# Kernel tuning notes

Measured on AMD Instinct MI355X. Metric: run time of the kernel, lower is better.

The kernel has to match this reference:

```python
import jax, jax.numpy as jnp
import numpy as np

STRIDES = (4, 8, 16)
LIMITS = np.array([[-1.0, 64.0], [64.0, 128.0], [128.0, 99999.0]], dtype=np.float32)


def _grid(H, W, stride):
    # FCOS grid: centers of stride-sized cells
    ys = (jnp.arange(H, dtype=jnp.float32) + 0.5) * stride
    xs = (jnp.arange(W, dtype=jnp.float32) + 0.5) * stride
    yy, xx = jnp.meshgrid(ys, xs, indexing='ij')
    return xx.reshape(-1), yy.reshape(-1)


def _flatten(p):
    B, C, H, W = p.shape
    return p.transpose(0, 2, 3, 1).reshape(B, H * W, C)


def compute_iou_score(pred, target):
    pl, pt, pr, pb = pred[..., 0], pred[..., 1], pred[..., 2], pred[..., 3]
    tl, tt, tr, tb = target[..., 0], target[..., 1], target[..., 2], target[..., 3]
    w_i = jnp.minimum(pl, tl) + jnp.minimum(pr, tr)
    h_i = jnp.minimum(pt, tt) + jnp.minimum(pb, tb)
    a_i = jnp.clip(w_i, 0) * jnp.clip(h_i, 0)
    a_p = (pl + pr) * (pt + pb)
    a_t = (tl + tr) * (tt + tb)
    a_u = a_t + a_p - a_i + 1e-07
    return jnp.clip(a_i / a_u, 0.0, 1.0)


def giou_loss(pred, target):
    pl, pt, pr, pb = pred[..., 0], pred[..., 1], pred[..., 2], pred[..., 3]
    tl, tt, tr, tb = target[..., 0], target[..., 1], target[..., 2], target[..., 3]
    w_i = jnp.minimum(pl, tl) + jnp.minimum(pr, tr)
    h_i = jnp.minimum(pt, tt) + jnp.minimum(pb, tb)
    a_i = jnp.clip(w_i, 0) * jnp.clip(h_i, 0)
    a_p = (pl + pr) * (pt + pb)
    a_t = (tl + tr) * (tt + tb)
    a_u = a_p + a_t - a_i + 1e-07
    iou = a_i / a_u
    w_e = jnp.maximum(pl, tl) + jnp.maximum(pr, tr)
    h_e = jnp.maximum(pt, tt) + jnp.maximum(pb, tb)
    a_e = jnp.clip(w_e, 0) * jnp.clip(h_e, 0) + 1e-07
    giou = iou - (a_e - a_u) / a_e
    return 1.0 - giou


def varifocal_loss(logits, gt_iou, alpha=0.75, gamma=2.0):
    p = jax.nn.sigmoid(logits)
    log_p = jax.nn.log_sigmoid(logits)       # log(sigmoid(x))
    log_np = jax.nn.log_sigmoid(-logits)     # log(1 - sigmoid(x))
    pos = gt_iou > 0
    pos_loss = -gt_iou * (gt_iou * log_p + (1.0 - gt_iou) * log_np)
    neg_loss = -alpha * p ** gamma * log_np
    return jnp.sum(jnp.where(pos, pos_loss, neg_loss))


def _fcos(cls_list, reg_list, gt_boxes):
    coords, lev = [], []
    for l, s in enumerate(STRIDES):
        H, W = cls_list[l].shape[2:]
        xx, yy = _grid(H, W, s)
        coords.append(jnp.stack([xx, yy], axis=1))
        lev.append(jnp.full((H * W,), l, dtype=jnp.int32))
    coords = jnp.concatenate(coords, 0)          # [N,2]
    lev = jnp.concatenate(lev, 0)
    lim = jnp.asarray(LIMITS)
    low, high = lim[lev, 0], lim[lev, 1]         # [N]
    pred_cls = jnp.concatenate([_flatten(p) for p in cls_list], 1)  # [B,N,1]
    pred_reg = jnp.concatenate([_flatten(p) for p in reg_list], 1)  # [B,N,4]
    xs, ys = coords[:, 0], coords[:, 1]

    def per_image(pcls, preg, boxes):
        # boxes: [M,4] xyxy
        l = xs[:, None] - boxes[None, :, 0]
        t = ys[:, None] - boxes[None, :, 1]
        r = boxes[None, :, 2] - xs[:, None]
        b = boxes[None, :, 3] - ys[:, None]
        rt = jnp.stack([l, t, r, b], axis=2)     # [N,M,4]
        in_box = jnp.min(rt, axis=2) > 0
        mx = jnp.max(rt, axis=2)
        in_lvl = (mx > low[:, None]) & (mx < high[:, None])
        areas = (boxes[:, 2] - boxes[:, 0]) * (boxes[:, 3] - boxes[:, 1])
        a = jnp.where(in_box & in_lvl, areas[None, :], jnp.inf)
        min_area = jnp.min(a, axis=1)
        idx = jnp.argmin(a, axis=1)              # min gt per location
        pos = jnp.isfinite(min_area)             # [N]
        matched = jnp.take_along_axis(rt, idx[:, None, None], axis=1)[:, 0, :]  # [N,4]
        iou = jax.lax.stop_gradient(compute_iou_score(preg, matched))
        cls_target = jnp.zeros_like(pcls).at[:, 0].set(jnp.where(pos, iou, 0.0))
        gl = giou_loss(preg, matched)
        reg_loss = jnp.sum(jnp.where(pos, gl, 0.0))
        cls_loss = varifocal_loss(pcls, cls_target)
        return cls_loss, reg_loss, jnp.sum(pos).astype(jnp.float32)

    cl, rl, npos = jax.vmap(per_image)(pred_cls, pred_reg, gt_boxes)
    B = pred_cls.shape[0]
    cls_sum, reg_sum = cl.sum(), rl.sum()
    navg = jnp.maximum(1.0, npos.sum() / B)
    return (cls_sum + reg_sum) / navg, cls_sum / navg, reg_sum / navg


def setup_inputs() -> dict:
    key = jax.random.key(0)
    ks = jax.random.split(key, 9)
    B, M = 16, 64
    cls0 = jax.random.normal(ks[0], (B, 1, 160, 160), dtype=jnp.float32)
    cls1 = jax.random.normal(ks[1], (B, 1, 80, 80), dtype=jnp.float32)
    cls2 = jax.random.normal(ks[2], (B, 1, 40, 40), dtype=jnp.float32)
    # positive ltrb offset predictions (as FCOS heads produce post-exp/relu)
    reg0 = jax.random.uniform(ks[3], (B, 4, 160, 160), dtype=jnp.float32) * 64.0 + 1.0
    reg1 = jax.random.uniform(ks[4], (B, 4, 80, 80), dtype=jnp.float32) * 64.0 + 1.0
    reg2 = jax.random.uniform(ks[5], (B, 4, 40, 40), dtype=jnp.float32) * 64.0 + 1.0
    xy = jax.random.uniform(ks[6], (B, M, 2), dtype=jnp.float32) * 540.0 + 5.0
    wh = jax.random.uniform(ks[7], (B, M, 2), dtype=jnp.float32) * 80.0 + 10.0
    gt_boxes = jnp.concatenate([xy, xy + wh], axis=-1)  # valid xyxy
    return {"cls0": cls0, "cls1": cls1, "cls2": cls2,
            "reg0": reg0, "reg1": reg1, "reg2": reg2, "gt_boxes": gt_boxes}


def reference(cls0, cls1, cls2, reg0, reg1, reg2, gt_boxes):
    total, cls_n, reg_n = _fcos([cls0, cls1, cls2], [reg0, reg1, reg2], gt_boxes)
    return total, cls_n, reg_n
```

## Files before the change

### kernel.cpp

```cpp
#include <hip/hip_runtime.h>
#include <math.h>

#define NL0 25600
#define NL1 6400
#define NL2 1600
#define MAXM 64
#define ANCH 2
#define TPB 256
#define APB (TPB * ANCH)
#define GX0 50
#define GX1 13
#define GX2 4
#define GX  (GX0 + GX1 + GX2)
#define NB 16
#define NPART (GX * NB)

__global__ __launch_bounds__(TPB, 1) void fcos_main(
    const float* __restrict__ cls0, const float* __restrict__ cls1,
    const float* __restrict__ cls2, const float* __restrict__ reg0,
    const float* __restrict__ reg1, const float* __restrict__ reg2,
    const float* __restrict__ boxes, int M, float* __restrict__ part)
{
    const int b  = blockIdx.y;
    const int lx = blockIdx.x;

    int ii0, W, hw; float s, low, high;
    const float* cb; const float* rb;
    if (lx < GX0) {
        ii0 = lx * APB;               W = 160; hw = NL0; s = 4.0f;
        low = -1.0f;  high = 64.0f;   cb = cls0; rb = reg0;
    } else if (lx < GX0 + GX1) {
        ii0 = (lx - GX0) * APB;       W = 80;  hw = NL1; s = 8.0f;
        low = 64.0f;  high = 128.0f;  cb = cls1; rb = reg1;
    } else {
        ii0 = (lx - GX0 - GX1) * APB; W = 40;  hw = NL2; s = 16.0f;
        low = 128.0f; high = 99999.0f; cb = cls2; rb = reg2;
    }

    const int r0 = ii0 / W;
    const int r1 = min(ii0 + APB - 1, hw - 1) / W;
    const float ymin = ((float)r0 + 0.5f) * s;
    const float ymax = ((float)r1 + 0.5f) * s;

    __shared__ float4   sbox[MAXM];
    __shared__ float4   cbox[MAXM];
    __shared__ unsigned cpk[MAXM];
    __shared__ int      scnt;

    if (threadIdx.x < 64) {
        const int j = threadIdx.x;
        float4 bx = make_float4(0.f, 0.f, 0.f, 0.f);
        unsigned pk = 0xFFFFFFFFu;
        bool keep = false;
        if (j < M) {
            bx = ((const float4*)boxes)[(size_t)b * M + j];
            const float bw = bx.z - bx.x, bh = bx.w - bx.y;
            const float area = bw * bh;
            pk = (__float_as_uint(area) & ~63u) | (unsigned)j;
            const float dmax = fmaxf(bw, bh);
            keep = (dmax > low) & (dmax < 2.0f * high) & (bx.y < ymax) & (bx.w > ymin);
        }
        sbox[j] = bx;
        const unsigned long long mk = __ballot(keep);
        if (keep) {
            const int pos = (int)__popcll(mk & ((1ull << j) - 1ull));
            cbox[pos] = bx;
            cpk[pos]  = pk;
        }
        if (j == 0) scnt = (int)__popcll(mk);
    }
    __syncthreads();
    const int cnt = scnt;

    float clsl = 0.0f, regl = 0.0f, posf = 0.0f;

    const int ii = ii0 + (int)threadIdx.x * ANCH;
    if (ii - ii0 < hw - ii0 && ii < hw) {
        const int h = ii / W, w = ii - h * W;
        const float x0 = ((float)w + 0.5f) * s;
        const float y  = ((float)h + 0.5f) * s;
        const float xk[ANCH] = { x0, x0 + s };

        const float* rp = rb + (size_t)b * 4 * hw + ii;
        const float2 pl2 = *(const float2*)(rp);
        const float2 pt2 = *(const float2*)(rp + hw);
        const float2 pr2 = *(const float2*)(rp + 2 * hw);
        const float2 pb2 = *(const float2*)(rp + 3 * hw);
        const float2 lg2 = *(const float2*)(cb + (size_t)b * hw + ii);
        const float plv[2] = { pl2.x, pl2.y };
        const float ptv[2] = { pt2.x, pt2.y };
        const float prv[2] = { pr2.x, pr2.y };
        const float pbv[2] = { pb2.x, pb2.y };
        const float lgv[2] = { lg2.x, lg2.y };

        unsigned best[ANCH] = { 0xFFFFFFFFu, 0xFFFFFFFFu };

        #pragma unroll 2
        for (int j = 0; j < cnt; ++j) {
            const float4 bx = cbox[j];
            const unsigned pk = cpk[j];
            const float t   = y - bx.y;
            const float bo  = bx.w - y;
            const float mtb = fminf(t, bo);
            const float xtb = fmaxf(t, bo);
            const float l0  = x0 - bx.x;
            const float r0f = bx.z - x0;
            #pragma unroll
            for (int k = 0; k < ANCH; ++k) {
                const float ks = (float)k * s;
                const float l = l0 + ks;
                const float r = r0f - ks;
                const float mn = fminf(fminf(l, r), mtb);
                const float mx = fmaxf(fmaxf(l, r), xtb);
                const bool ok = (mn > 0.0f) & (mx > low) & (mx < high);
                const unsigned cand = ok ? pk : 0xFFFFFFFFu;
                best[k] = min(best[k], cand);
            }
        }

        #pragma unroll
        for (int k = 0; k < ANCH; ++k) {
            const bool pos = (best[k] != 0xFFFFFFFFu);
            const int idx = (int)(best[k] & 63u);
            const float4 tbx = sbox[idx];
            const float xc = xk[k];
            const float tl = xc - tbx.x, tt = y - tbx.y;
            const float tr = tbx.z - xc, tb = tbx.w - y;

            const float pl = plv[k], pt = ptv[k], pr = prv[k], pb = pbv[k];

            const float w_i = fminf(pl, tl) + fminf(pr, tr);
            const float h_i = fminf(pt, tt) + fminf(pb, tb);
            const float a_i = fmaxf(w_i, 0.0f) * fmaxf(h_i, 0.0f);
            const float a_p = (pl + pr) * (pt + pb);
            const float a_t = (tl + tr) * (tt + tb);
            const float a_u = a_p + a_t - a_i + 1e-7f;
            const float iou_raw = a_i / a_u;

            const float w_e = fmaxf(pl, tl) + fmaxf(pr, tr);
            const float h_e = fmaxf(pt, tt) + fmaxf(pb, tb);
            const float a_e = fmaxf(w_e, 0.0f) * fmaxf(h_e, 0.0f) + 1e-7f;
            const float gl = 1.0f - (iou_raw - (a_e - a_u) / a_e);

            regl += pos ? gl : 0.0f;
            posf += pos ? 1.0f : 0.0f;
            const float gt_iou = pos ? fminf(fmaxf(iou_raw, 0.0f), 1.0f) : 0.0f;

            const float logit = lgv[k];
            const float e   = expf(-fabsf(logit));
            const float l1p = log1pf(e);
            const float log_p  = fminf(logit, 0.0f) - l1p;
            const float log_np = fminf(-logit, 0.0f) - l1p;
            const float p = 1.0f / (1.0f + expf(-logit));
            if (gt_iou > 0.0f)
                clsl += -gt_iou * (gt_iou * log_p + (1.0f - gt_iou) * log_np);
            else
                clsl += -0.75f * p * p * log_np;
        }
    }

    float v0 = clsl, v1 = regl, v2 = posf;
    #pragma unroll
    for (int off = 32; off > 0; off >>= 1) {
        v0 += __shfl_down(v0, off);
        v1 += __shfl_down(v1, off);
        v2 += __shfl_down(v2, off);
    }
    __shared__ float red[3][TPB / 64];
    const int lane = threadIdx.x & 63;
    const int wv   = threadIdx.x >> 6;
    if (lane == 0) { red[0][wv] = v0; red[1][wv] = v1; red[2][wv] = v2; }
    __syncthreads();
    if (threadIdx.x == 0) {
        float s0 = 0, s1 = 0, s2 = 0;
        #pragma unroll
        for (int wvi = 0; wvi < TPB / 64; ++wvi) { s0 += red[0][wvi]; s1 += red[1][wvi]; s2 += red[2][wvi]; }
        const int p = blockIdx.y * GX + blockIdx.x;
        part[p]             = s0;
        part[NPART + p]     = s1;
        part[2 * NPART + p] = s2;
    }
}

__global__ __launch_bounds__(TPB) void fcos_final(
    const float* __restrict__ part, float* __restrict__ out, int B)
{
    float s0 = 0.0f, s1 = 0.0f, s2 = 0.0f;
    for (int i = threadIdx.x; i < NPART; i += TPB) {
        s0 += part[i];
        s1 += part[NPART + i];
        s2 += part[2 * NPART + i];
    }
    #pragma unroll
    for (int off = 32; off > 0; off >>= 1) {
        s0 += __shfl_down(s0, off);
        s1 += __shfl_down(s1, off);
        s2 += __shfl_down(s2, off);
    }
    __shared__ float red[3][TPB / 64];
    const int lane = threadIdx.x & 63;
    const int wv   = threadIdx.x >> 6;
    if (lane == 0) { red[0][wv] = s0; red[1][wv] = s1; red[2][wv] = s2; }
    __syncthreads();
    if (threadIdx.x == 0) {
        float cls_sum = 0, reg_sum = 0, npos = 0;
        #pragma unroll
        for (int wvi = 0; wvi < TPB / 64; ++wvi) {
            cls_sum += red[0][wvi]; reg_sum += red[1][wvi]; npos += red[2][wvi];
        }
        const float navg = fmaxf(1.0f, npos / (float)B);
        out[0] = (cls_sum + reg_sum) / navg;
        out[1] = cls_sum / navg;
        out[2] = reg_sum / navg;
    }
}

extern "C" void kernel_launch(void* const* d_in, const int* in_sizes, int n_in,
                              void* d_out, int out_size, void* d_ws, size_t ws_size,
                              hipStream_t stream) {
    const float* cls0 = (const float*)d_in[0];
    const float* cls1 = (const float*)d_in[1];
    const float* cls2 = (const float*)d_in[2];
    const float* reg0 = (const float*)d_in[3];
    const float* reg1 = (const float*)d_in[4];
    const float* reg2 = (const float*)d_in[5];
    const float* boxes = (const float*)d_in[6];

    const int B = in_sizes[0] / NL0;
    const int M = in_sizes[6] / (4 * B);

    float* part = (float*)d_ws;

    dim3 grid(GX, B);
    fcos_main<<<grid, TPB, 0, stream>>>(cls0, cls1, cls2, reg0, reg1, reg2,
                                        boxes, M, part);
    fcos_final<<<1, TPB, 0, stream>>>(part, (float*)d_out, B);
}
```

Measured before the change: 79.19 us.

## Fuse final reduction into main kernel via last-block atomic counters

Replaces the separate final reduction kernel with a last-block-done scheme. Each block publishes its partials and bumps a per-batch counter. The last block per batch reduces that batch and bumps a global counter, and the last of those writes the outputs. This removes a dependent kernel launch but adds a memset of the counters and atomic traffic.

```diff
diff --git a/kernel.cpp b/kernel.cpp
--- a/kernel.cpp
+++ b/kernel.cpp
@@ -15,11 +15,16 @@
 #define NB 16
 #define NPART (GX * NB)
 
-__global__ __launch_bounds__(TPB, 1) void fcos_main(
+#define CNT_OFF  12928
+#define CNT_LINES 17
+#define ISUM_OFF (CNT_OFF + CNT_LINES * 128)
+
+__global__ __launch_bounds__(TPB, 1) void fcos_fused(
     const float* __restrict__ cls0, const float* __restrict__ cls1,
     const float* __restrict__ cls2, const float* __restrict__ reg0,
     const float* __restrict__ reg1, const float* __restrict__ reg2,
-    const float* __restrict__ boxes, int M, float* __restrict__ part)
+    const float* __restrict__ boxes, int M, int B,
+    float* part, unsigned* cnts, float* isum, float* out)
 {
     const int b  = blockIdx.y;
     const int lx = blockIdx.x;
@@ -75,7 +80,7 @@
     float clsl = 0.0f, regl = 0.0f, posf = 0.0f;
 
     const int ii = ii0 + (int)threadIdx.x * ANCH;
-    if (ii - ii0 < hw - ii0 && ii < hw) {
+    if (ii < hw) {
         const int h = ii / W, w = ii - h * W;
         const float x0 = ((float)w + 0.5f) * s;
         const float y  = ((float)h + 0.5f) * s;
@@ -159,6 +164,11 @@
         }
     }
 
+    __shared__ float red[3][TPB / 64];
+    __shared__ int sflag;
+    const int lane = threadIdx.x & 63;
+    const int wv   = threadIdx.x >> 6;
+
     float v0 = clsl, v1 = regl, v2 = posf;
     #pragma unroll
     for (int off = 32; off > 0; off >>= 1) {
@@ -166,52 +176,73 @@
         v1 += __shfl_down(v1, off);
         v2 += __shfl_down(v2, off);
     }
-    __shared__ float red[3][TPB / 64];
-    const int lane = threadIdx.x & 63;
-    const int wv   = threadIdx.x >> 6;
     if (lane == 0) { red[0][wv] = v0; red[1][wv] = v1; red[2][wv] = v2; }
     __syncthreads();
     if (threadIdx.x == 0) {
         float s0 = 0, s1 = 0, s2 = 0;
         #pragma unroll
         for (int wvi = 0; wvi < TPB / 64; ++wvi) { s0 += red[0][wvi]; s1 += red[1][wvi]; s2 += red[2][wvi]; }
-        const int p = blockIdx.y * GX + blockIdx.x;
-        part[p]             = s0;
-        part[NPART + p]     = s1;
-        part[2 * NPART + p] = s2;
-    }
-}
-
-__global__ __launch_bounds__(TPB) void fcos_final(
-    const float* __restrict__ part, float* __restrict__ out, int B)
-{
-    float s0 = 0.0f, s1 = 0.0f, s2 = 0.0f;
-    for (int i = threadIdx.x; i < NPART; i += TPB) {
-        s0 += part[i];
-        s1 += part[NPART + i];
-        s2 += part[2 * NPART + i];
-    }
-    #pragma unroll
-    for (int off = 32; off > 0; off >>= 1) {
-        s0 += __shfl_down(s0, off);
-        s1 += __shfl_down(s1, off);
-        s2 += __shfl_down(s2, off);
-    }
-    __shared__ float red[3][TPB / 64];
-    const int lane = threadIdx.x & 63;
-    const int wv   = threadIdx.x >> 6;
-    if (lane == 0) { red[0][wv] = s0; red[1][wv] = s1; red[2][wv] = s2; }
+        const int p = b * GX + lx;
+        __hip_atomic_store(&part[p],             s0, __ATOMIC_RELAXED, __HIP_MEMORY_SCOPE_AGENT);
+        __hip_atomic_store(&part[NPART + p],     s1, __ATOMIC_RELAXED, __HIP_MEMORY_SCOPE_AGENT);
+        __hip_atomic_store(&part[2 * NPART + p], s2, __ATOMIC_RELAXED, __HIP_MEMORY_SCOPE_AGENT);
+        const unsigned r = __hip_atomic_fetch_add(&cnts[b * 32], 1u,
+                                                  __ATOMIC_ACQ_REL, __HIP_MEMORY_SCOPE_AGENT);
+        sflag = (r == GX - 1);
+    }
     __syncthreads();
-    if (threadIdx.x == 0) {
-        float cls_sum = 0, reg_sum = 0, npos = 0;
+
+    if (sflag) {
+        float u0 = 0, u1 = 0, u2 = 0;
+        if (threadIdx.x < GX) {
+            const int q = b * GX + threadIdx.x;
+            u0 = __hip_atomic_load(&part[q],             __ATOMIC_RELAXED, __HIP_MEMORY_SCOPE_AGENT);
+            u1 = __hip_atomic_load(&part[NPART + q],     __ATOMIC_RELAXED, __HIP_MEMORY_SCOPE_AGENT);
+            u2 = __hip_atomic_load(&part[2 * NPART + q], __ATOMIC_RELAXED, __HIP_MEMORY_SCOPE_AGENT);
+        }
         #pragma unroll
-        for (int wvi = 0; wvi < TPB / 64; ++wvi) {
-            cls_sum += red[0][wvi]; reg_sum += red[1][wvi]; npos += red[2][wvi];
-        }
-        const float navg = fmaxf(1.0f, npos / (float)B);
-        out[0] = (cls_sum + reg_sum) / navg;
-        out[1] = cls_sum / navg;
-        out[2] = reg_sum / navg;
+        for (int off = 32; off > 0; off >>= 1) {
+            u0 += __shfl_down(u0, off);
+            u1 += __shfl_down(u1, off);
+            u2 += __shfl_down(u2, off);
+        }
+        if (lane == 0) { red[0][wv] = u0; red[1][wv] = u1; red[2][wv] = u2; }
+        __syncthreads();
+        if (threadIdx.x == 0) {
+            float t0 = 0, t1 = 0, t2 = 0;
+            #pragma unroll
+            for (int wvi = 0; wvi < TPB / 64; ++wvi) { t0 += red[0][wvi]; t1 += red[1][wvi]; t2 += red[2][wvi]; }
+            __hip_atomic_store(&isum[b],      t0, __ATOMIC_RELAXED, __HIP_MEMORY_SCOPE_AGENT);
+            __hip_atomic_store(&isum[16 + b], t1, __ATOMIC_RELAXED, __HIP_MEMORY_SCOPE_AGENT);
+            __hip_atomic_store(&isum[32 + b], t2, __ATOMIC_RELAXED, __HIP_MEMORY_SCOPE_AGENT);
+            const unsigned g = __hip_atomic_fetch_add(&cnts[16 * 32], 1u,
+                                                      __ATOMIC_ACQ_REL, __HIP_MEMORY_SCOPE_AGENT);
+            sflag = (g == (unsigned)B - 1);
+        }
+        __syncthreads();
+
+        if (sflag) {
+            if (threadIdx.x < 64) {
+                float f0 = 0, f1 = 0, f2 = 0;
+                if (threadIdx.x < B) {
+                    f0 = __hip_atomic_load(&isum[threadIdx.x],      __ATOMIC_RELAXED, __HIP_MEMORY_SCOPE_AGENT);
+                    f1 = __hip_atomic_load(&isum[16 + threadIdx.x], __ATOMIC_RELAXED, __HIP_MEMORY_SCOPE_AGENT);
+                    f2 = __hip_atomic_load(&isum[32 + threadIdx.x], __ATOMIC_RELAXED, __HIP_MEMORY_SCOPE_AGENT);
+                }
+                #pragma unroll
+                for (int off = 32; off > 0; off >>= 1) {
+                    f0 += __shfl_down(f0, off);
+                    f1 += __shfl_down(f1, off);
+                    f2 += __shfl_down(f2, off);
+                }
+                if (threadIdx.x == 0) {
+                    const float navg = fmaxf(1.0f, f2 / (float)B);
+                    out[0] = (f0 + f1) / navg;
+                    out[1] = f0 / navg;
+                    out[2] = f1 / navg;
+                }
+            }
+        }
     }
 }
 
@@ -229,10 +260,14 @@
     const int B = in_sizes[0] / NL0;
     const int M = in_sizes[6] / (4 * B);
 
-    float* part = (float*)d_ws;
+    float*    part = (float*)d_ws;
+    unsigned* cnts = (unsigned*)((char*)d_ws + CNT_OFF);
+    float*    isum = (float*)((char*)d_ws + ISUM_OFF);
+
+    hipMemsetAsync(cnts, 0, CNT_LINES * 128, stream);
 
     dim3 grid(GX, B);
-    fcos_main<<<grid, TPB, 0, stream>>>(cls0, cls1, cls2, reg0, reg1, reg2,
-                                        boxes, M, part);
-    fcos_final<<<1, TPB, 0, stream>>>(part, (float*)d_out, B);
+    fcos_fused<<<grid, TPB, 0, stream>>>(cls0, cls1, cls2, reg0, reg1, reg2,
+                                         boxes, M, B, part, cnts, isum,
+                                         (float*)d_out);
 }
```

New measurement: 90.81 us. 14.7% more time.
